# Performance work log

Measured on AMD Instinct MI355X. Metric: run time of the kernel, lower is better.

Reference implementation:

```python
import jax, jax.numpy as jnp
from jax import lax
import numpy as np

T = 8  # num_temp_tokens (init kwarg, closed over as a static constant)


def setup_inputs() -> dict:
    key = jax.random.key(0)
    k1, k2, k3, k4, k5 = jax.random.split(key, 5)
    B, N, C = 16, 197, 768
    bt = B * T
    x = jax.random.normal(k1, (bt, N, C), dtype=jnp.float32)
    # routing conv1d: C -> 3C, kernel 3 (original inits to zero; small random for testing)
    a_weight = jax.random.normal(k2, (3 * C, C, 3), dtype=jnp.float32) * 0.02
    a_bias = jax.random.normal(k3, (3 * C,), dtype=jnp.float32) * 0.02
    # main linear weight (out_channels=3C, in_channels=C) and bias
    weight = jax.random.normal(k4, (3 * C, C), dtype=jnp.float32) * 0.02
    bias = jax.random.normal(k5, (3 * C,), dtype=jnp.float32) * 0.02
    return {"x": x, "a_weight": a_weight, "a_bias": a_bias, "weight": weight, "bias": bias}


def reference(x, a_weight, a_bias, weight, bias):
    bt, n, c = x.shape
    b = bt // T
    xr = x.reshape(b, T, n, c)                      # (b, t, n, c)
    # routing: conv1d over T on the CLS token, then +1
    cls = jnp.transpose(xr[:, :, 0, :], (0, 2, 1))  # (b, c, t)
    r = lax.conv_general_dilated(
        cls, a_weight, window_strides=(1,), padding=[(1, 1)],
        dimension_numbers=("NCH", "OIH", "NCH"),
    ) + a_bias[None, :, None] + 1.0                 # (b, 3c, t)
    s = jnp.transpose(r, (0, 2, 1)).reshape(b, T, 3, c)   # per-(b,t) q/k/v c_in scales
    Wr = weight.reshape(3, c, c)                    # (3, c_out, c_in)
    br = bias.reshape(3, c)
    # scale input channels per (b, t, group), then batched GEMM
    xs = xr[:, :, None, :, :] * s[:, :, :, None, :]       # (b, t, 3, n, c)
    out = jnp.einsum("goi,btgni->btgon", Wr, xs)          # (b, t, 3, c_out, n)
    out = out + (br[None, None] * s)[..., None]           # bias also modulated by scales
    return out.reshape(bt, 3 * c, n)                # (b*t, 3c, n) == torch output layout
```

## Files before the change

kernel.cpp:

```cpp
#include <hip/hip_runtime.h>

#define NTOK 197
#define C 768
#define C3 2304
#define BM 128
#define BK 32
#define PK 40
#define NT 13

typedef __attribute__((ext_vector_type(4))) float f32x4;
typedef __attribute__((ext_vector_type(8))) short bf16x8;

__device__ __forceinline__ ushort f2bf(float f){
  uint u = __float_as_uint(f);
  u += 0x7fffu + ((u >> 16) & 1u);
  return (ushort)(u >> 16);
}
__device__ __forceinline__ uint pack2(float a, float b){
  return (uint)f2bf(a) | ((uint)f2bf(b) << 16);
}
__device__ __forceinline__ float bfu2f(uint u){ return __uint_as_float(u << 16); }

__global__ __launch_bounds__(256)
void conv_scales(const float* __restrict__ x, const float* __restrict__ aw,
                 const float* __restrict__ ab, float* __restrict__ s_ws)
{
  __shared__ __align__(16) float cls[10][C];
  __shared__ float partial[64][4][8];
  const int oc  = blockIdx.x;
  const int b   = blockIdx.y;
  const int tid = threadIdx.x;

  for (int task = tid; task < 1920; task += 256){
    int row = task / 192, c4 = task % 192;
    float4 v = {0.f,0.f,0.f,0.f};
    if (row >= 1 && row <= 8)
      v = *reinterpret_cast<const float4*>(x + (size_t)(b*8 + row - 1)*NTOK*C + c4*4);
    *reinterpret_cast<float4*>(&cls[row][c4*4]) = v;
  }
  __syncthreads();

  const int ol = tid >> 2, part = tid & 3;
  const int o_full = oc*64 + ol;
  float acc[8];
  #pragma unroll
  for (int t=0;t<8;t++) acc[t]=0.f;
  const float* awrow = aw + (size_t)o_full*2304;

  for (int i = part*192; i < part*192 + 192; i += 4){
    const float* ap = awrow + i*3;
    float4 a0 = *reinterpret_cast<const float4*>(ap);
    float4 a1 = *reinterpret_cast<const float4*>(ap+4);
    float4 a2 = *reinterpret_cast<const float4*>(ap+8);
    float awf[12] = {a0.x,a0.y,a0.z,a0.w, a1.x,a1.y,a1.z,a1.w, a2.x,a2.y,a2.z,a2.w};
    float4 cv[10];
    #pragma unroll
    for (int t=0;t<10;t++) cv[t] = *reinterpret_cast<const float4*>(&cls[t][i]);
    #pragma unroll
    for (int e=0;e<4;e++){
      float w0 = awf[e*3+0], w1 = awf[e*3+1], w2 = awf[e*3+2];
      #pragma unroll
      for (int t=0;t<8;t++){
        const float* c0 = reinterpret_cast<const float*>(&cv[t]);
        const float* c1 = reinterpret_cast<const float*>(&cv[t+1]);
        const float* c2 = reinterpret_cast<const float*>(&cv[t+2]);
        acc[t] += w0*c0[e] + w1*c1[e] + w2*c2[e];
      }
    }
  }
  #pragma unroll
  for (int t=0;t<8;t++) partial[ol][part][t] = acc[t];
  __syncthreads();

  for (int idx = tid; idx < 512; idx += 256){
    int o_l = idx >> 3, t = idx & 7;
    float v = partial[o_l][0][t] + partial[o_l][1][t]
            + partial[o_l][2][t] + partial[o_l][3][t]
            + ab[oc*64 + o_l] + 1.0f;
    s_ws[(size_t)(b*8 + t)*C3 + oc*64 + o_l] = v;
  }
}

__global__ void cvt_bf16(const float* __restrict__ in, ushort* __restrict__ outp, int n4)
{
  int stride = gridDim.x * blockDim.x;
  for (int i = blockIdx.x*blockDim.x + threadIdx.x; i < n4; i += stride){
    float4 v = reinterpret_cast<const float4*>(in)[i];
    ushort4 o;
    o.x = f2bf(v.x); o.y = f2bf(v.y); o.z = f2bf(v.z); o.w = f2bf(v.w);
    reinterpret_cast<ushort4*>(outp)[i] = o;
  }
}

template<bool XBF>
__global__ __launch_bounds__(512)
void gemm_kernel(const float* __restrict__ x, const ushort* __restrict__ xbf,
                 const ushort* __restrict__ wbf, const float* __restrict__ s_ws,
                 const float* __restrict__ bias, float* __restrict__ out)
{
  __shared__ __align__(16) ushort A_lds[BM*PK];
  __shared__ __align__(16) ushort B_lds[208*PK];
  const int ot  = blockIdx.x;
  const int g   = blockIdx.y;
  const int bt  = blockIdx.z;
  const int tid = threadIdx.x;
  const int w = tid >> 6, lane = tid & 63;
  const int l15 = lane & 15, lq = lane >> 4;

  const float*  srow  = s_ws + (size_t)bt*C3 + (size_t)g*C;
  const ushort* wrow  = wbf + ((size_t)g*C + (size_t)ot*BM)*C;
  const float*  xrow  = x   + (size_t)bt*NTOK*C;
  const ushort* xbrow = xbf + (size_t)bt*NTOK*C;

  f32x4 acc[NT];
  #pragma unroll
  for (int j=0;j<NT;j++) acc[j] = (f32x4){0.f,0.f,0.f,0.f};

  const int ar = tid >> 2, ac = tid & 3;

  for (int k0 = 0; k0 < C; k0 += BK){
    {
      uint4 wv = *reinterpret_cast<const uint4*>(wrow + (size_t)ar*C + k0 + ac*8);
      const float* sv = srow + k0 + ac*8;
      float4 s0 = *reinterpret_cast<const float4*>(sv);
      float4 s1 = *reinterpret_cast<const float4*>(sv+4);
      uint4 av;
      av.x = pack2(bfu2f(wv.x & 0xffffu)*s0.x, bfu2f(wv.x >> 16)*s0.y);
      av.y = pack2(bfu2f(wv.y & 0xffffu)*s0.z, bfu2f(wv.y >> 16)*s0.w);
      av.z = pack2(bfu2f(wv.z & 0xffffu)*s1.x, bfu2f(wv.z >> 16)*s1.y);
      av.w = pack2(bfu2f(wv.w & 0xffffu)*s1.z, bfu2f(wv.w >> 16)*s1.w);
      *reinterpret_cast<uint4*>(&A_lds[ar*PK + ac*8]) = av;
    }
    #pragma unroll
    for (int it = 0; it < 2; ++it){
      int task = tid + it*512;
      if (task < 832){
        int r = task >> 2, cc = task & 3;
        uint4 bv = {0u,0u,0u,0u};
        if (r < NTOK){
          if (XBF){
            bv = *reinterpret_cast<const uint4*>(xbrow + (size_t)r*C + k0 + cc*8);
          } else {
            const float* p = xrow + (size_t)r*C + k0 + cc*8;
            float4 lo = *reinterpret_cast<const float4*>(p);
            float4 hi = *reinterpret_cast<const float4*>(p+4);
            bv.x = pack2(lo.x, lo.y); bv.y = pack2(lo.z, lo.w);
            bv.z = pack2(hi.x, hi.y); bv.w = pack2(hi.z, hi.w);
          }
        }
        *reinterpret_cast<uint4*>(&B_lds[r*PK + cc*8]) = bv;
      }
    }
    __syncthreads();

    bf16x8 a = *reinterpret_cast<const bf16x8*>(&A_lds[(w*16 + l15)*PK + lq*8]);
    #pragma unroll
    for (int j=0;j<NT;j++){
      bf16x8 b = *reinterpret_cast<const bf16x8*>(&B_lds[(j*16 + l15)*PK + lq*8]);
      acc[j] = __builtin_amdgcn_mfma_f32_16x16x32_bf16(a, b, acc[j], 0, 0, 0);
    }
    __syncthreads();
  }

  const int obase = ot*BM + w*16 + lq*4;
  float bs[4];
  #pragma unroll
  for (int r=0;r<4;r++)
    bs[r] = bias[g*C + obase + r] * srow[obase + r];
  #pragma unroll
  for (int j=0;j<NT;j++){
    int n = j*16 + l15;
    if (n < NTOK){
      #pragma unroll
      for (int r=0;r<4;r++)
        out[((size_t)bt*C3 + g*C + obase + r)*NTOK + n] = acc[j][r] + bs[r];
    }
  }
}

extern "C" void kernel_launch(void* const* d_in, const int* in_sizes, int n_in,
                              void* d_out, int out_size, void* d_ws, size_t ws_size,
                              hipStream_t stream)
{
  const float* x        = (const float*)d_in[0];
  const float* a_weight = (const float*)d_in[1];
  const float* a_bias   = (const float*)d_in[2];
  const float* weight   = (const float*)d_in[3];
  const float* bias     = (const float*)d_in[4];
  float* out = (float*)d_out;

  char* ws = (char*)d_ws;
  float*  s_ws = (float*)ws;
  ushort* wbf  = (ushort*)(ws + 1179648);
  ushort* xbf  = (ushort*)(ws + 4718592);
  const bool use_xbf = ws_size >= (size_t)43450368;

  conv_scales<<<dim3(36,16), 256, 0, stream>>>(x, a_weight, a_bias, s_ws);
  cvt_bf16<<<dim3(1728), 256, 0, stream>>>(weight, wbf, 442368);
  if (use_xbf){
    cvt_bf16<<<dim3(4096), 256, 0, stream>>>(x, xbf, 4841472);
    gemm_kernel<true><<<dim3(6,3,128), 512, 0, stream>>>(x, xbf, wbf, s_ws, bias, out);
  } else {
    gemm_kernel<false><<<dim3(6,3,128), 512, 0, stream>>>(x, xbf, wbf, s_ws, bias, out);
  }
}
```

Baseline: 563.3 us.

## Restructure GEMM with 2x13 wave tiles, direct-to-LDS loads, swizzled grid; merge conversions

```diff
diff --git a/kernel.cpp b/kernel.cpp
--- a/kernel.cpp
+++ b/kernel.cpp
@@ -3,13 +3,15 @@
 #define NTOK 197
 #define C 768
 #define C3 2304
-#define BM 128
 #define BK 32
 #define PK 40
 #define NT 13
+#define CPAD 772
+#define AWP 200
 
 typedef __attribute__((ext_vector_type(4))) float f32x4;
 typedef __attribute__((ext_vector_type(8))) short bf16x8;
+typedef unsigned int u32;
 
 __device__ __forceinline__ ushort f2bf(float f){
   uint u = __float_as_uint(f);
@@ -21,15 +23,39 @@
 }
 __device__ __forceinline__ float bfu2f(uint u){ return __uint_as_float(u << 16); }
 
+__device__ __forceinline__ void glds16(ushort* lds, const ushort* gsrc){
+  __builtin_amdgcn_global_load_lds((const __attribute__((address_space(1))) u32*)gsrc,
+                                   (__attribute__((address_space(3))) u32*)lds, 16, 0, 0);
+}
+
+#define N4_W 442368
+#define N4_X 4841472
+__global__ void cvt_all(const float* __restrict__ w, const float* __restrict__ x,
+                        ushort* __restrict__ wbf, ushort* __restrict__ xbf)
+{
+  const int n4 = N4_W + N4_X;
+  int stride = gridDim.x * blockDim.x;
+  for (int i = blockIdx.x*blockDim.x + threadIdx.x; i < n4; i += stride){
+    const float4* src; ushort4* dst;
+    if (i < N4_W){ src = reinterpret_cast<const float4*>(w) + i;
+                   dst = reinterpret_cast<ushort4*>(wbf) + i; }
+    else         { src = reinterpret_cast<const float4*>(x) + (i - N4_W);
+                   dst = reinterpret_cast<ushort4*>(xbf) + (i - N4_W); }
+    float4 v = *src;
+    ushort4 o;
+    o.x = f2bf(v.x); o.y = f2bf(v.y); o.z = f2bf(v.z); o.w = f2bf(v.w);
+    *dst = o;
+  }
+}
+
 __global__ __launch_bounds__(256)
-void conv_scales(const float* __restrict__ x, const float* __restrict__ aw,
-                 const float* __restrict__ ab, float* __restrict__ s_ws)
-{
-  __shared__ __align__(16) float cls[10][C];
-  __shared__ float partial[64][4][8];
-  const int oc  = blockIdx.x;
-  const int b   = blockIdx.y;
-  const int tid = threadIdx.x;
+void conv3(const float* __restrict__ x, const float* __restrict__ aw,
+           const float* __restrict__ ab, float* __restrict__ s_ws)
+{
+  __shared__ __align__(16) float  cls[10][CPAD];
+  __shared__ __align__(16) ushort awt[64*AWP];
+  __shared__ float partial[64][4][9];
+  const int oc = blockIdx.x, b = blockIdx.y, tid = threadIdx.x;
 
   for (int task = tid; task < 1920; task += 256){
     int row = task / 192, c4 = task % 192;
@@ -38,67 +64,161 @@
       v = *reinterpret_cast<const float4*>(x + (size_t)(b*8 + row - 1)*NTOK*C + c4*4);
     *reinterpret_cast<float4*>(&cls[row][c4*4]) = v;
   }
+
+  const int o_l = tid >> 2, part = tid & 3;
+  float acc[8];
+  #pragma unroll
+  for (int t=0;t<8;t++) acc[t]=0.f;
+
+  for (int it = 0; it < 12; ++it){
+    const int i0 = it*64;
+    #pragma unroll
+    for (int j = 0; j < 12; ++j){
+      int task = tid + j*256;
+      int r = task / 48, c4 = task % 48;
+      float4 v = *reinterpret_cast<const float4*>(aw + (size_t)(oc*64 + r)*C3 + i0*3 + c4*4);
+      uint2 pk; pk.x = pack2(v.x, v.y); pk.y = pack2(v.z, v.w);
+      *reinterpret_cast<uint2*>(&awt[r*AWP + c4*4]) = pk;
+    }
+    __syncthreads();
+
+    #pragma unroll
+    for (int qq = 0; qq < 4; ++qq){
+      const int i_loc = part*16 + qq*4;
+      const int ib = i0 + i_loc;
+      float4 cv[10];
+      #pragma unroll
+      for (int t=0;t<10;t++) cv[t] = *reinterpret_cast<const float4*>(&cls[t][ib]);
+      float wv[4][3];
+      #pragma unroll
+      for (int e=0;e<4;e++){
+        #pragma unroll
+        for (int dk=0;dk<3;dk++)
+          wv[e][dk] = bfu2f((uint)awt[o_l*AWP + (i_loc+e)*3 + dk]);
+      }
+      #pragma unroll
+      for (int e=0;e<4;e++){
+        #pragma unroll
+        for (int dk=0;dk<3;dk++){
+          const float wf = wv[e][dk];
+          #pragma unroll
+          for (int t=0;t<8;t++){
+            const float* cp = reinterpret_cast<const float*>(&cv[t+dk]);
+            acc[t] += wf * cp[e];
+          }
+        }
+      }
+    }
+    __syncthreads();
+  }
+
+  #pragma unroll
+  for (int t=0;t<8;t++) partial[o_l][part][t] = acc[t];
   __syncthreads();
 
-  const int ol = tid >> 2, part = tid & 3;
-  const int o_full = oc*64 + ol;
-  float acc[8];
-  #pragma unroll
-  for (int t=0;t<8;t++) acc[t]=0.f;
-  const float* awrow = aw + (size_t)o_full*2304;
-
-  for (int i = part*192; i < part*192 + 192; i += 4){
-    const float* ap = awrow + i*3;
-    float4 a0 = *reinterpret_cast<const float4*>(ap);
-    float4 a1 = *reinterpret_cast<const float4*>(ap+4);
-    float4 a2 = *reinterpret_cast<const float4*>(ap+8);
-    float awf[12] = {a0.x,a0.y,a0.z,a0.w, a1.x,a1.y,a1.z,a1.w, a2.x,a2.y,a2.z,a2.w};
-    float4 cv[10];
-    #pragma unroll
-    for (int t=0;t<10;t++) cv[t] = *reinterpret_cast<const float4*>(&cls[t][i]);
-    #pragma unroll
-    for (int e=0;e<4;e++){
-      float w0 = awf[e*3+0], w1 = awf[e*3+1], w2 = awf[e*3+2];
-      #pragma unroll
-      for (int t=0;t<8;t++){
-        const float* c0 = reinterpret_cast<const float*>(&cv[t]);
-        const float* c1 = reinterpret_cast<const float*>(&cv[t+1]);
-        const float* c2 = reinterpret_cast<const float*>(&cv[t+2]);
-        acc[t] += w0*c0[e] + w1*c1[e] + w2*c2[e];
+  for (int idx = tid; idx < 512; idx += 256){
+    int o = idx >> 3, t = idx & 7;
+    float v = partial[o][0][t] + partial[o][1][t]
+            + partial[o][2][t] + partial[o][3][t]
+            + ab[oc*64 + o] + 1.0f;
+    s_ws[(size_t)(b*8 + t)*C3 + oc*64 + o] = v;
+  }
+}
+
+__global__ __launch_bounds__(256)
+void gemm3(const ushort* __restrict__ wbf, const ushort* __restrict__ xbf,
+           const float* __restrict__ s_ws, const float* __restrict__ bias,
+           float* __restrict__ out)
+{
+  __shared__ __align__(16) ushort A_lds[128*BK];
+  __shared__ __align__(16) ushort B_lds[208*BK];
+
+  const int lid  = blockIdx.x;
+  const int work = (lid & 7)*288 + (lid >> 3);
+  const int bt   = work / 18;
+  const int rem  = work - bt*18;
+  const int g    = rem / 6;
+  const int mt   = rem - g*6;
+
+  const int tid = threadIdx.x, w = tid >> 6, lane = tid & 63;
+  const int l15 = lane & 15, lq = lane >> 4;
+
+  const float*  srow = s_ws + (size_t)bt*C3 + (size_t)g*C;
+  const ushort* Ap   = wbf + ((size_t)g*C + (size_t)mt*128)*C;
+  const ushort* xb   = xbf + (size_t)bt*NTOK*C;
+
+  const int arow  = tid >> 1;
+  const int acol  = (tid & 1) * 16;
+
+  f32x4 acc[2][13];
+  #pragma unroll
+  for (int i=0;i<2;i++)
+    #pragma unroll
+    for (int j=0;j<13;j++) acc[i][j] = (f32x4){0.f,0.f,0.f,0.f};
+
+  for (int k0 = 0; k0 < C; k0 += BK){
+    {
+      const ushort* wp = Ap + (size_t)arow*C + k0 + acol;
+      uint4 w0 = *reinterpret_cast<const uint4*>(wp);
+      uint4 w1 = *reinterpret_cast<const uint4*>(wp + 8);
+      const float* sp = srow + k0 + acol;
+      float4 s0 = *reinterpret_cast<const float4*>(sp);
+      float4 s1 = *reinterpret_cast<const float4*>(sp+4);
+      float4 s2 = *reinterpret_cast<const float4*>(sp+8);
+      float4 s3 = *reinterpret_cast<const float4*>(sp+12);
+      uint4 o0, o1;
+      o0.x = pack2(bfu2f(w0.x & 0xffffu)*s0.x, bfu2f(w0.x >> 16)*s0.y);
+      o0.y = pack2(bfu2f(w0.y & 0xffffu)*s0.z, bfu2f(w0.y >> 16)*s0.w);
+      o0.z = pack2(bfu2f(w0.z & 0xffffu)*s1.x, bfu2f(w0.z >> 16)*s1.y);
+      o0.w = pack2(bfu2f(w0.w & 0xffffu)*s1.z, bfu2f(w0.w >> 16)*s1.w);
+      o1.x = pack2(bfu2f(w1.x & 0xffffu)*s2.x, bfu2f(w1.x >> 16)*s2.y);
+      o1.y = pack2(bfu2f(w1.y & 0xffffu)*s2.z, bfu2f(w1.y >> 16)*s2.w);
+      o1.z = pack2(bfu2f(w1.z & 0xffffu)*s3.x, bfu2f(w1.z >> 16)*s3.y);
+      o1.w = pack2(bfu2f(w1.w & 0xffffu)*s3.z, bfu2f(w1.w >> 16)*s3.w);
+      *reinterpret_cast<uint4*>(&A_lds[arow*BK + acol    ]) = o0;
+      *reinterpret_cast<uint4*>(&A_lds[arow*BK + acol + 8]) = o1;
+    }
+    for (int e = w; e < 13; e += 4){
+      glds16(&B_lds[e*512], xb + (size_t)(e*16 + (lane>>2))*C + k0 + (lane&3)*8);
+    }
+    __syncthreads();
+
+    bf16x8 a0 = *reinterpret_cast<const bf16x8*>(&A_lds[(w*32      + l15)*BK + lq*8]);
+    bf16x8 a1 = *reinterpret_cast<const bf16x8*>(&A_lds[(w*32 + 16 + l15)*BK + lq*8]);
+    #pragma unroll
+    for (int nf=0; nf<13; nf++){
+      bf16x8 b = *reinterpret_cast<const bf16x8*>(&B_lds[(nf*16 + l15)*BK + lq*8]);
+      acc[0][nf] = __builtin_amdgcn_mfma_f32_16x16x32_bf16(a0, b, acc[0][nf], 0, 0, 0);
+      acc[1][nf] = __builtin_amdgcn_mfma_f32_16x16x32_bf16(a1, b, acc[1][nf], 0, 0, 0);
+    }
+    __syncthreads();
+  }
+
+  #pragma unroll
+  for (int mf=0; mf<2; mf++){
+    const int o0 = mt*128 + w*32 + mf*16 + lq*4;
+    float bs[4];
+    #pragma unroll
+    for (int r=0;r<4;r++)
+      bs[r] = bias[g*C + o0 + r] * srow[o0 + r];
+    #pragma unroll
+    for (int nf=0; nf<13; nf++){
+      int n = nf*16 + l15;
+      if (n < NTOK){
+        #pragma unroll
+        for (int r=0;r<4;r++)
+          out[((size_t)bt*C3 + g*C + o0 + r)*NTOK + n] = acc[mf][nf][r] + bs[r];
       }
     }
   }
-  #pragma unroll
-  for (int t=0;t<8;t++) partial[ol][part][t] = acc[t];
-  __syncthreads();
-
-  for (int idx = tid; idx < 512; idx += 256){
-    int o_l = idx >> 3, t = idx & 7;
-    float v = partial[o_l][0][t] + partial[o_l][1][t]
-            + partial[o_l][2][t] + partial[o_l][3][t]
-            + ab[oc*64 + o_l] + 1.0f;
-    s_ws[(size_t)(b*8 + t)*C3 + oc*64 + o_l] = v;
-  }
-}
-
-__global__ void cvt_bf16(const float* __restrict__ in, ushort* __restrict__ outp, int n4)
-{
-  int stride = gridDim.x * blockDim.x;
-  for (int i = blockIdx.x*blockDim.x + threadIdx.x; i < n4; i += stride){
-    float4 v = reinterpret_cast<const float4*>(in)[i];
-    ushort4 o;
-    o.x = f2bf(v.x); o.y = f2bf(v.y); o.z = f2bf(v.z); o.w = f2bf(v.w);
-    reinterpret_cast<ushort4*>(outp)[i] = o;
-  }
-}
-
-template<bool XBF>
+}
+
 __global__ __launch_bounds__(512)
-void gemm_kernel(const float* __restrict__ x, const ushort* __restrict__ xbf,
-                 const ushort* __restrict__ wbf, const float* __restrict__ s_ws,
-                 const float* __restrict__ bias, float* __restrict__ out)
-{
-  __shared__ __align__(16) ushort A_lds[BM*PK];
+void gemm_fb(const float* __restrict__ x, const ushort* __restrict__ wbf,
+             const float* __restrict__ s_ws, const float* __restrict__ bias,
+             float* __restrict__ out)
+{
+  __shared__ __align__(16) ushort A_lds[128*PK];
   __shared__ __align__(16) ushort B_lds[208*PK];
   const int ot  = blockIdx.x;
   const int g   = blockIdx.y;
@@ -108,9 +228,8 @@
   const int l15 = lane & 15, lq = lane >> 4;
 
   const float*  srow  = s_ws + (size_t)bt*C3 + (size_t)g*C;
-  const ushort* wrow  = wbf + ((size_t)g*C + (size_t)ot*BM)*C;
+  const ushort* wrow  = wbf + ((size_t)g*C + (size_t)ot*128)*C;
   const float*  xrow  = x   + (size_t)bt*NTOK*C;
-  const ushort* xbrow = xbf + (size_t)bt*NTOK*C;
 
   f32x4 acc[NT];
   #pragma unroll
@@ -138,15 +257,11 @@
         int r = task >> 2, cc = task & 3;
         uint4 bv = {0u,0u,0u,0u};
         if (r < NTOK){
-          if (XBF){
-            bv = *reinterpret_cast<const uint4*>(xbrow + (size_t)r*C + k0 + cc*8);
-          } else {
-            const float* p = xrow + (size_t)r*C + k0 + cc*8;
-            float4 lo = *reinterpret_cast<const float4*>(p);
-            float4 hi = *reinterpret_cast<const float4*>(p+4);
-            bv.x = pack2(lo.x, lo.y); bv.y = pack2(lo.z, lo.w);
-            bv.z = pack2(hi.x, hi.y); bv.w = pack2(hi.z, hi.w);
-          }
+          const float* p = xrow + (size_t)r*C + k0 + cc*8;
+          float4 lo = *reinterpret_cast<const float4*>(p);
+          float4 hi = *reinterpret_cast<const float4*>(p+4);
+          bv.x = pack2(lo.x, lo.y); bv.y = pack2(lo.z, lo.w);
+          bv.z = pack2(hi.x, hi.y); bv.w = pack2(hi.z, hi.w);
         }
         *reinterpret_cast<uint4*>(&B_lds[r*PK + cc*8]) = bv;
       }
@@ -162,7 +277,7 @@
     __syncthreads();
   }
 
-  const int obase = ot*BM + w*16 + lq*4;
+  const int obase = ot*128 + w*16 + lq*4;
   float bs[4];
   #pragma unroll
   for (int r=0;r<4;r++)
@@ -178,6 +293,17 @@
   }
 }
 
+__global__ void cvt_w_only(const float* __restrict__ in, ushort* __restrict__ outp, int n4)
+{
+  int stride = gridDim.x * blockDim.x;
+  for (int i = blockIdx.x*blockDim.x + threadIdx.x; i < n4; i += stride){
+    float4 v = reinterpret_cast<const float4*>(in)[i];
+    ushort4 o;
+    o.x = f2bf(v.x); o.y = f2bf(v.y); o.z = f2bf(v.z); o.w = f2bf(v.w);
+    reinterpret_cast<ushort4*>(outp)[i] = o;
+  }
+}
+
 extern "C" void kernel_launch(void* const* d_in, const int* in_sizes, int n_in,
                               void* d_out, int out_size, void* d_ws, size_t ws_size,
                               hipStream_t stream)
@@ -193,14 +319,15 @@
   float*  s_ws = (float*)ws;
   ushort* wbf  = (ushort*)(ws + 1179648);
   ushort* xbf  = (ushort*)(ws + 4718592);
-  const bool use_xbf = ws_size >= (size_t)43450368;
-
-  conv_scales<<<dim3(36,16), 256, 0, stream>>>(x, a_weight, a_bias, s_ws);
-  cvt_bf16<<<dim3(1728), 256, 0, stream>>>(weight, wbf, 442368);
-  if (use_xbf){
-    cvt_bf16<<<dim3(4096), 256, 0, stream>>>(x, xbf, 4841472);
-    gemm_kernel<true><<<dim3(6,3,128), 512, 0, stream>>>(x, xbf, wbf, s_ws, bias, out);
+  const size_t NEED_FULL = 43483136;
+
+  if (ws_size >= NEED_FULL){
+    cvt_all<<<dim3(2048), 256, 0, stream>>>(weight, x, wbf, xbf);
+    conv3<<<dim3(36,16), 256, 0, stream>>>(x, a_weight, a_bias, s_ws);
+    gemm3<<<dim3(2304), 256, 0, stream>>>(wbf, xbf, s_ws, bias, out);
   } else {
-    gemm_kernel<false><<<dim3(6,3,128), 512, 0, stream>>>(x, xbf, wbf, s_ws, bias, out);
-  }
-}
+    cvt_w_only<<<dim3(1728), 256, 0, stream>>>(weight, wbf, 442368);
+    conv3<<<dim3(36,16), 256, 0, stream>>>(x, a_weight, a_bias, s_ws);
+    gemm_fb<<<dim3(6,3,128), 512, 0, stream>>>(x, wbf, s_ws, bias, out);
+  }
+}
```

New measurement: 650.6 us. 1.16x slower.
